# Kernel tuning notes

Hardware: AMD Instinct MI355X
Metric: run time of the kernel (lower is better)

## Reference

```python
import jax, jax.numpy as jnp
import numpy as np

C = 128                  # stem_dim
CONV_DIM = C * C * 3 * 3 # 147456
B, T = 32, 30
N_CH = 1024
N_ANS = 32               # n_answers + 1
V = 44

UNARY = [4,10,11,12,13,14,15,16,17,18,19,20,21,22,23,24,25,29,30,31,32,33,34,35,36,37,38,39,40,41,43]
BINARY = [5,6,7,8,9,26,27,28,42]
SCENE_TOK = 4

_kind = np.zeros(V, np.int32)   # 0=special, 1=scene, 2=unary, 3=binary
_uidx = np.zeros(V, np.int32)
_bidx = np.zeros(V, np.int32)
for _j, _t in enumerate(UNARY):
    _kind[_t] = 2; _uidx[_t] = _j
for _j, _t in enumerate(BINARY):
    _kind[_t] = 3; _bidx[_t] = _j
_kind[SCENE_TOK] = 1
KIND_T, U_T, B_T = jnp.array(_kind), jnp.array(_uidx), jnp.array(_bidx)


def conv3x3(x, w):  # x [N,C,H,W], w [O,I,3,3], pad=1
    return jax.lax.conv_general_dilated(x, w, (1, 1), ((1, 1), (1, 1)),
                                        dimension_numbers=('NCHW', 'OIHW', 'NCHW'))


def conv1x1(x, w):
    return jax.lax.conv_general_dilated(x, w, (1, 1), ((0, 0), (0, 0)),
                                        dimension_numbers=('NCHW', 'OIHW', 'NCHW'))

# per-sample weights: vmap conv over batch
_bconv = jax.vmap(lambda x, w: conv3x3(x[None], w)[0])


def exec_unary(x, w1, w2):
    return jax.nn.relu(_bconv(jax.nn.relu(_bconv(x, w1)), w2))


def exec_binary(x1, x2, w1, w2, w3):
    h = jax.nn.relu(_bconv(jnp.concatenate([x1, x2], axis=1), w1))
    h = jax.nn.relu(_bconv(h, w2))
    return jax.nn.relu(_bconv(h, w3))


def setup_inputs() -> dict:
    key = jax.random.key(0)
    ks = jax.random.split(key, 10)
    std = 1.0 / float(np.sqrt(CONV_DIM))
    r = lambda k, shp, s: jax.random.normal(k, shp, jnp.float32) * s
    return {
        'feats': jax.random.normal(ks[0], (B, N_CH, 14, 14), jnp.float32),
        'programs': jax.random.randint(ks[1], (B, T), 0, V, dtype=jnp.int32),
        'stem_w1': r(ks[2], (C, N_CH, 3, 3), 0.02),
        'stem_b1': jnp.zeros((C,), jnp.float32),
        'stem_w2': r(ks[3], (C, C, 3, 3), 0.05),
        'stem_b2': jnp.zeros((C,), jnp.float32),
        'mem_u': jax.random.uniform(ks[4], (31, 2 * CONV_DIM), jnp.float32, -std, std),
        'mem_b': jax.random.uniform(ks[5], (9, 4 * CONV_DIM), jnp.float32, -std, std),
        'cls_w': r(ks[6], (512, C, 1, 1), 0.05),
        'cls_b': jnp.zeros((512,), jnp.float32),
        'fc1_w': r(ks[7], (1024, 512 * 7 * 7), 0.01),
        'fc1_b': jnp.zeros((1024,), jnp.float32),
        'fc2_w': r(ks[8], (N_ANS, 1024), 0.03),
        'fc2_b': jnp.zeros((N_ANS,), jnp.float32),
    }


def reference(feats, programs, stem_w1, stem_b1, stem_w2, stem_b2, mem_u, mem_b,
              cls_w, cls_b, fc1_w, fc1_b, fc2_w, fc2_b):
    # stem: conv3x3 -> relu -> conv3x3 -> relu
    h = jax.nn.relu(conv3x3(feats, stem_w1) + stem_b1[None, :, None, None])
    feat = jax.nn.relu(conv3x3(h, stem_w2) + stem_b2[None, :, None, None])  # [B,C,14,14]

    def step(carry, tok):  # tok [B] int32
        out, saved = carry
        kind = KIND_T[tok]                           # [B]
        uread = mem_u[U_T[tok]]                      # [B, 2*CONV_DIM] one-hot memory read
        w1 = uread[:, :CONV_DIM].reshape(-1, C, C, 3, 3)
        w2 = uread[:, CONV_DIM:].reshape(-1, C, C, 3, 3)
        bread = mem_b[B_T[tok]]                      # [B, 4*CONV_DIM]
        bw1 = bread[:, :2 * CONV_DIM].reshape(-1, C, 2 * C, 3, 3)
        bw2 = bread[:, 2 * CONV_DIM:3 * CONV_DIM].reshape(-1, C, C, 3, 3)
        bw3 = bread[:, 3 * CONV_DIM:].reshape(-1, C, C, 3, 3)
        is_scene = (kind == 1)[:, None, None, None]
        u_in = jnp.where(is_scene, feat, out)        # scene runs on stem features
        u_out = exec_unary(u_in, w1, w2)
        b_out = exec_binary(out, saved, bw1, bw2, bw3)
        k4 = kind[:, None, None, None]
        new_saved = jnp.where(is_scene, out, saved)  # scene saves current output
        new_out = jnp.where(k4 == 0, out, jnp.where(k4 == 3, b_out, u_out))
        return (new_out, new_saved), None

    toks_rev = programs[:, ::-1].T.astype(jnp.int32)  # [T,B] reversed program
    (out, _), _ = jax.lax.scan(step, (feat, jnp.zeros_like(feat)), toks_rev)

    # classifier: conv1x1 -> relu -> maxpool2 -> flatten -> fc -> relu -> fc
    h = jax.nn.relu(conv1x1(out, cls_w) + cls_b[None, :, None, None])
    h = jax.lax.reduce_window(h, -jnp.inf, jax.lax.max, (1, 1, 2, 2), (1, 1, 2, 2), 'VALID')
    h = h.reshape(h.shape[0], -1)                     # [B, 512*7*7]
    h = jax.nn.relu(h @ fc1_w.T + fc1_b)
    return h @ fc2_w.T + fc2_b                        # [B, N_ANS]
```

## Files before the change

kernel.cpp:

```cpp
#include <hip/hip_runtime.h>


#define NSTEP 30
#define CD 147456
#define P 196
#define FSZ 25088
#define LROW 18
#define LBUF (272*LROW)

typedef __attribute__((ext_vector_type(8))) short short8;
typedef __attribute__((ext_vector_type(16))) float f32x16;

__constant__ int KIND_TBL[44] = {
  0,0,0,0,1,3,3,3,3,3, 2,2,2,2,2,2,2,2,2,2,
  2,2,2,2,2,2,3,3,3,2, 2,2,2,2,2,2,2,2,2,2, 2,2,3,2};
__constant__ int MIDX_TBL[44] = {
  0,0,0,0,0,0,1,2,3,4, 1,2,3,4,5,6,7,8,9,10,
  11,12,13,14,15,16,5,6,7,17, 18,19,20,21,22,23,24,25,26,27, 28,29,8,30};

__device__ __forceinline__ uint32_t bf16_rne(float x) {
  uint32_t u = __float_as_uint(x);
  return (u + 0x7fffu + ((u >> 16) & 1u)) >> 16;
}
__device__ __forceinline__ uint32_t pack_hl(float x) {
  uint32_t h = bf16_rne(x);
  float rest = x - __uint_as_float(h << 16);
  uint32_t l = bf16_rne(rest);
  return (h << 16) | l;
}
__device__ __forceinline__ float ld_sc0(const float* p) {
  return __hip_atomic_load(p, __ATOMIC_RELAXED, __HIP_MEMORY_SCOPE_AGENT);
}

__device__ __forceinline__ void bbar(int* __restrict__ ctr, int target) {
  __syncthreads();
  if (threadIdx.x == 0) {
    __hip_atomic_fetch_add(ctr, 1, __ATOMIC_RELEASE, __HIP_MEMORY_SCOPE_AGENT);
    while (__hip_atomic_load(ctr, __ATOMIC_ACQUIRE, __HIP_MEMORY_SCOPE_AGENT) < target)
      __builtin_amdgcn_s_sleep(2);
  }
  __syncthreads();
}

__global__ void __launch_bounds__(256) repack_kernel(
    const float* __restrict__ sw1, const float* __restrict__ sw2,
    const float* __restrict__ mu, const float* __restrict__ mb,
    uint32_t* __restrict__ Wp)
{
  const int blk = blockIdx.x;
  const int C = blk / 9, tap = blk % 9;
  const float* src; int nic, lc;
  if (C < 64)       { src = sw1; nic = 1024; lc = C; }
  else if (C < 72)  { src = sw2; nic = 128;  lc = C - 64; }
  else if (C < 568) { int u = (C - 72) >> 4, r = (C - 72) & 15;
                      src = mu + (size_t)u * 2 * CD + (size_t)(r >> 3) * CD;
                      nic = 128; lc = r & 7; }
  else              { int j = (C - 568) >> 5, r = (C - 568) & 31;
                      const float* base = mb + (size_t)j * 4 * CD;
                      if (r < 16)      { src = base;                  nic = 256; lc = r; }
                      else if (r < 24) { src = base + 2 * (size_t)CD; nic = 128; lc = r - 16; }
                      else             { src = base + 3 * (size_t)CD; nic = 128; lc = r - 24; } }
  const int mt = threadIdx.x >> 6, lane = threadIdx.x & 63;
  const int oc = mt * 32 + (lane & 31);
  const int ic0 = lc * 16 + (lane >> 5) * 8;
  uint32_t hw[4], lw[4];
#pragma unroll
  for (int pr = 0; pr < 4; ++pr) {
    uint32_t hh[2], ll[2];
#pragma unroll
    for (int e = 0; e < 2; ++e) {
      float x = src[((size_t)oc * nic + (ic0 + pr * 2 + e)) * 9 + tap];
      uint32_t h = bf16_rne(x);
      float rest = x - __uint_as_float(h << 16);
      hh[e] = h; ll[e] = bf16_rne(rest);
    }
    hw[pr] = hh[0] | (hh[1] << 16);
    lw[pr] = ll[0] | (ll[1] << 16);
  }
  uint32_t* dstb = Wp + (size_t)blk * 2048;
  *(uint4*)(dstb + (mt * 2 + 0) * 256 + lane * 4) = make_uint4(hw[0], hw[1], hw[2], hw[3]);
  *(uint4*)(dstb + (mt * 2 + 1) * 256 + lane * 4) = make_uint4(lw[0], lw[1], lw[2], lw[3]);
}

union BU { uint32_t u[4]; uint4 v; short8 s8; };

__device__ __forceinline__ void load_wchunk(const uint32_t* __restrict__ wb,
                                            BU* wh, BU* wl) {
#pragma unroll
  for (int t = 0; t < 9; ++t) {
    wh[t].v = *(const uint4*)(wb + t * 2048);
    wl[t].v = *(const uint4*)(wb + t * 2048 + 256);
  }
}

__device__ __forceinline__ void mfma_chunk(const uint32_t* __restrict__ sb,
                                           int pwbase, const BU* wh, const BU* wl,
                                           f32x16& acc) {
  const int TAPOFF[9] = {0, 1, 2, 16, 17, 18, 32, 33, 34};
#pragma unroll
  for (int tap = 0; tap < 9; ++tap) {
    const int pw = pwbase + TAPOFF[tap] * LROW;
    uint2 q0 = *(const uint2*)(sb + pw);
    uint2 q1 = *(const uint2*)(sb + pw + 2);
    uint2 q2 = *(const uint2*)(sb + pw + 4);
    uint2 q3 = *(const uint2*)(sb + pw + 6);
    BU Bh, Bl;
    Bh.u[0] = __builtin_amdgcn_perm(q0.y, q0.x, 0x07060302u);
    Bh.u[1] = __builtin_amdgcn_perm(q1.y, q1.x, 0x07060302u);
    Bh.u[2] = __builtin_amdgcn_perm(q2.y, q2.x, 0x07060302u);
    Bh.u[3] = __builtin_amdgcn_perm(q3.y, q3.x, 0x07060302u);
    Bl.u[0] = __builtin_amdgcn_perm(q0.y, q0.x, 0x05040100u);
    Bl.u[1] = __builtin_amdgcn_perm(q1.y, q1.x, 0x05040100u);
    Bl.u[2] = __builtin_amdgcn_perm(q2.y, q2.x, 0x05040100u);
    Bl.u[3] = __builtin_amdgcn_perm(q3.y, q3.x, 0x05040100u);
    acc = __builtin_amdgcn_mfma_f32_32x32x16_bf16(wh[tap].s8, Bh.s8, acc, 0, 0, 0);
    acc = __builtin_amdgcn_mfma_f32_32x32x16_bf16(wh[tap].s8, Bl.s8, acc, 0, 0, 0);
    acc = __builtin_amdgcn_mfma_f32_32x32x16_bf16(wl[tap].s8, Bh.s8, acc, 0, 0, 0);
  }
}

__device__ __forceinline__ void conv_run(
    uint32_t sbuf[2][LBUF],
    const float* __restrict__ in0, const float* __restrict__ in1, int split, int nc,
    int C0, int mt,
    const uint32_t* __restrict__ Wp, const float* __restrict__ bias,
    float* __restrict__ dst, float* __restrict__ dst2, float* __restrict__ zb,
    const int* imgoff)
{
  const int tid = threadIdx.x;
  const int w = tid >> 6, lane = tid & 63, l31 = lane & 31, kq = lane >> 5;
  const int ic16 = tid >> 5, pl = tid & 31;
  const int pwbase = (32 * w + l31) * LROW + kq * 8;
  const bool cw = (w < 7);
  const uint32_t* wbase = Wp + (size_t)C0 * 9 * 2048 + (mt * 2) * 256 + lane * 4;

  f32x16 acc;
#pragma unroll
  for (int i = 0; i < 16; ++i) acc[i] = 0.f;

  BU whA[9], wlA[9], whB[9], wlB[9];
  if (cw) load_wchunk(wbase, whA, wlA);
  {
    const float* src = in0 + (size_t)ic16 * P;
#pragma unroll
    for (int i = 0; i < 9; ++i) {
      int p = pl + 32 * i;
      if (p < 272) {
        int off = imgoff[i];
        float x = (off >= 0) ? ld_sc0(src + off) : 0.f;
        sbuf[0][p * LROW + ic16] = pack_hl(x);
      }
    }
  }
  __syncthreads();

  int c = 0;
  while (true) {
    {
      const bool more = c + 1 < nc;
      float sv[9];
      if (more) {
        const int cn = c + 1;
        const float* src = (cn < split) ? in0 + (size_t)(cn * 16 + ic16) * P
                                        : in1 + (size_t)((cn - split) * 16 + ic16) * P;
#pragma unroll
        for (int i = 0; i < 9; ++i) {
          int off = imgoff[i];
          sv[i] = (off >= 0) ? ld_sc0(src + off) : 0.f;
        }
        if (cw) load_wchunk(wbase + (size_t)(c + 1) * 9 * 2048, whB, wlB);
      }
      if (cw) mfma_chunk(&sbuf[c & 1][0], pwbase, whA, wlA, acc);
      if (more) {
#pragma unroll
        for (int i = 0; i < 9; ++i) {
          int p = pl + 32 * i;
          if (p < 272) sbuf[(c + 1) & 1][p * LROW + ic16] = pack_hl(sv[i]);
        }
      }
      __syncthreads();
      if (++c >= nc) break;
    }
    {
      const bool more = c + 1 < nc;
      float sv[9];
      if (more) {
        const int cn = c + 1;
        const float* src = (cn < split) ? in0 + (size_t)(cn * 16 + ic16) * P
                                        : in1 + (size_t)((cn - split) * 16 + ic16) * P;
#pragma unroll
        for (int i = 0; i < 9; ++i) {
          int off = imgoff[i];
          sv[i] = (off >= 0) ? ld_sc0(src + off) : 0.f;
        }
        if (cw) load_wchunk(wbase + (size_t)(c + 1) * 9 * 2048, whA, wlA);
      }
      if (cw) mfma_chunk(&sbuf[c & 1][0], pwbase, whB, wlB, acc);
      if (more) {
#pragma unroll
        for (int i = 0; i < 9; ++i) {
          int p = pl + 32 * i;
          if (p < 272) sbuf[(c + 1) & 1][p * LROW + ic16] = pack_hl(sv[i]);
        }
      }
      __syncthreads();
      if (++c >= nc) break;
    }
  }

  if (cw) {
    const int ox = l31 & 15, oy = 2 * w + (l31 >> 4);
    if (ox < 14) {
#pragma unroll
      for (int reg = 0; reg < 16; ++reg) {
        int row = (reg & 3) + 8 * (reg >> 2) + 4 * kq;
        int oc = mt * 32 + row;
        float v = acc[reg];
        if (bias) v += bias[row];
        v = fmaxf(v, 0.f);
        dst[(size_t)oc * P + oy * 14 + ox] = v;
        if (dst2) dst2[(size_t)oc * P + oy * 14 + ox] = v;
        if (zb)   zb[(size_t)oc * P + oy * 14 + ox] = 0.f;
      }
    }
  }
}

__global__ void __launch_bounds__(512, 2) persist_kernel(
    const float* __restrict__ feats, const int* __restrict__ progs,
    const float* __restrict__ sb1, const float* __restrict__ sb2,
    const uint32_t* __restrict__ Wp,
    float* __restrict__ feat, float* __restrict__ outb, float* __restrict__ saved,
    float* __restrict__ h1, float* __restrict__ h2, int* __restrict__ ctr)
{
  __shared__ uint32_t s_act[2][LBUF];
  const int tid = threadIdx.x;
  const int b = blockIdx.x >> 2;
  const int mt = blockIdx.x & 3;
  const size_t bo = (size_t)b * FSZ;
  int* myctr = ctr + b * 32;
  int phase = 0;

  int imgoff[9];
#pragma unroll
  for (int i = 0; i < 9; ++i) {
    int p = (tid & 31) + 32 * i;
    int row = p >> 4, col = p & 15;
    imgoff[i] = (p < 272 && row >= 1 && row <= 14 && col >= 1 && col <= 14)
                ? (row - 1) * 14 + (col - 1) : -1;
  }

  conv_run(s_act, feats + (size_t)b * 1024 * P, nullptr, 1 << 28, 64, 0, mt, Wp,
           sb1 + mt * 32, h1 + bo, nullptr, nullptr, imgoff);
  bbar(myctr, ++phase * 4);
  conv_run(s_act, h1 + bo, nullptr, 1 << 28, 8, 64, mt, Wp,
           sb2 + mt * 32, feat + bo, outb + bo, saved + bo, imgoff);
  bbar(myctr, ++phase * 4);

  for (int s = 0; s < NSTEP; ++s) {
    int tok = progs[b * NSTEP + (NSTEP - 1 - s)];
    int kind = KIND_TBL[tok], mi = MIDX_TBL[tok];
    if (kind == 0) continue;
    if (kind == 1) {
      const size_t so = bo + (size_t)mt * 32 * P;
      for (int i = tid; i < 32 * P; i += 512)
        saved[so + i] = ld_sc0(&outb[so + i]);
      int C0 = 72 + mi * 16;
      conv_run(s_act, feat + bo, nullptr, 1 << 28, 8, C0, mt, Wp, nullptr,
               h1 + bo, nullptr, nullptr, imgoff);
      bbar(myctr, ++phase * 4);
      conv_run(s_act, h1 + bo, nullptr, 1 << 28, 8, C0 + 8, mt, Wp, nullptr,
               outb + bo, nullptr, nullptr, imgoff);
      bbar(myctr, ++phase * 4);
    } else if (kind == 2) {
      int C0 = 72 + mi * 16;
      conv_run(s_act, outb + bo, nullptr, 1 << 28, 8, C0, mt, Wp, nullptr,
               h1 + bo, nullptr, nullptr, imgoff);
      bbar(myctr, ++phase * 4);
      conv_run(s_act, h1 + bo, nullptr, 1 << 28, 8, C0 + 8, mt, Wp, nullptr,
               outb + bo, nullptr, nullptr, imgoff);
      bbar(myctr, ++phase * 4);
    } else {
      int C0 = 568 + mi * 32;
      conv_run(s_act, outb + bo, saved + bo, 8, 16, C0, mt, Wp, nullptr,
               h1 + bo, nullptr, nullptr, imgoff);
      bbar(myctr, ++phase * 4);
      conv_run(s_act, h1 + bo, nullptr, 1 << 28, 8, C0 + 16, mt, Wp, nullptr,
               h2 + bo, nullptr, nullptr, imgoff);
      bbar(myctr, ++phase * 4);
      conv_run(s_act, h2 + bo, nullptr, 1 << 28, 8, C0 + 24, mt, Wp, nullptr,
               outb + bo, nullptr, nullptr, imgoff);
      bbar(myctr, ++phase * 4);
    }
  }
}

__global__ void __launch_bounds__(256) cls_pool_kernel(
    const float* __restrict__ x, const float* __restrict__ Wc,
    const float* __restrict__ bc, float* __restrict__ hB)
{
  const int b = blockIdx.y, og = blockIdx.x;
  const int oc0 = og * 64;
  __shared__ float s[16 * P];
  const float* xb = x + (size_t)b * FSZ;
  const int tid = threadIdx.x;
  float acc[13][4];
#pragma unroll
  for (int k = 0; k < 13; ++k) { acc[k][0] = acc[k][1] = acc[k][2] = acc[k][3] = 0.f; }
  for (int c0 = 0; c0 < 128; c0 += 16) {
    __syncthreads();
    for (int i = tid; i < 16 * P; i += 256) s[i] = xb[(size_t)c0 * P + i];
    __syncthreads();
#pragma unroll
    for (int k = 0; k < 13; ++k) {
      const int idx = k * 256 + tid;
      if (idx < 64 * 49) {
        const int oc = oc0 + idx / 49, pp = idx % 49;
        const int py = pp / 7, px = pp % 7;
        const int b0 = 2 * py * 14 + 2 * px, b1 = b0 + 14;
        const float* wr = Wc + (size_t)oc * 128 + c0;
#pragma unroll
        for (int ic = 0; ic < 16; ++ic) {
          const float w = wr[ic];
          const float* sp = s + ic * P;
          const float2 r0 = *(const float2*)(sp + b0);
          const float2 r1 = *(const float2*)(sp + b1);
          acc[k][0] = fmaf(w, r0.x, acc[k][0]);
          acc[k][1] = fmaf(w, r0.y, acc[k][1]);
          acc[k][2] = fmaf(w, r1.x, acc[k][2]);
          acc[k][3] = fmaf(w, r1.y, acc[k][3]);
        }
      }
    }
  }
#pragma unroll
  for (int k = 0; k < 13; ++k) {
    const int idx = k * 256 + tid;
    if (idx < 64 * 49) {
      const int oc = oc0 + idx / 49, pp = idx % 49;
      const float m = fmaxf(fmaxf(acc[k][0], acc[k][1]), fmaxf(acc[k][2], acc[k][3]));
      hB[(size_t)b * 25088 + (size_t)oc * 49 + pp] = fmaxf(m + bc[oc], 0.f);
    }
  }
}

__global__ void __launch_bounds__(256) transpose_kernel(
    const float* __restrict__ hB, float* __restrict__ hT)
{
  __shared__ float t[256 * 33];
  const int k0 = blockIdx.x * 256;
  const int tid = threadIdx.x;
  for (int b = 0; b < 32; ++b)
    t[tid * 33 + b] = hB[(size_t)b * 25088 + k0 + tid];
  __syncthreads();
  for (int i = tid; i < 256 * 32; i += 256) {
    const int k = i >> 5, b = i & 31;
    hT[(size_t)(k0 + k) * 32 + b] = t[k * 33 + b];
  }
}

__global__ void __launch_bounds__(256) fc1_kernel(
    const float* __restrict__ hT, const float* __restrict__ W,
    const float* __restrict__ bias, float* __restrict__ o)
{
  const int b = threadIdx.x & 31, j = threadIdx.x >> 5;
  const int oc = blockIdx.x * 4 + (j & 3);
  const int kh = j >> 2;
  const float* wr = W + (size_t)oc * 25088 + (size_t)kh * 12544;
  const float* ht = hT + (size_t)kh * 12544 * 32;
  float acc = 0.f;
  for (int k = 0; k < 12544; k += 4) {
    const float4 w4 = *(const float4*)(wr + k);
    acc = fmaf(ht[(size_t)(k + 0) * 32 + b], w4.x, acc);
    acc = fmaf(ht[(size_t)(k + 1) * 32 + b], w4.y, acc);
    acc = fmaf(ht[(size_t)(k + 2) * 32 + b], w4.z, acc);
    acc = fmaf(ht[(size_t)(k + 3) * 32 + b], w4.w, acc);
  }
  __shared__ float red[8][32];
  red[j][b] = acc;
  __syncthreads();
  if (j < 4)
    o[(size_t)b * 1024 + oc] = fmaxf(red[j][b] + red[j + 4][b] + bias[oc], 0.f);
}

__global__ void __launch_bounds__(256) fc2_kernel(
    const float* __restrict__ h, const float* __restrict__ W,
    const float* __restrict__ bias, float* __restrict__ out)
{
  const int i = blockIdx.x * 256 + threadIdx.x;
  const int b = i >> 5, oo = i & 31;
  const float* wr = W + (size_t)oo * 1024;
  const float* hr = h + (size_t)b * 1024;
  float acc = bias[oo];
  for (int k = 0; k < 1024; k += 4) {
    const float4 w4 = *(const float4*)(wr + k);
    const float4 h4 = *(const float4*)(hr + k);
    acc = fmaf(h4.x, w4.x, acc);
    acc = fmaf(h4.y, w4.y, acc);
    acc = fmaf(h4.z, w4.z, acc);
    acc = fmaf(h4.w, w4.w, acc);
  }
  out[i] = acc;
}

extern "C" void kernel_launch(void* const* d_in, const int* in_sizes, int n_in,
                              void* d_out, int out_size, void* d_ws, size_t ws_size,
                              hipStream_t stream) {
  const float* feats   = (const float*)d_in[0];
  const int*   progs   = (const int*)  d_in[1];
  const float* stem_w1 = (const float*)d_in[2];
  const float* stem_b1 = (const float*)d_in[3];
  const float* stem_w2 = (const float*)d_in[4];
  const float* stem_b2 = (const float*)d_in[5];
  const float* mem_u   = (const float*)d_in[6];
  const float* mem_b   = (const float*)d_in[7];
  const float* cls_w   = (const float*)d_in[8];
  const float* cls_b   = (const float*)d_in[9];
  const float* fc1_w   = (const float*)d_in[10];
  const float* fc1_b   = (const float*)d_in[11];
  const float* fc2_w   = (const float*)d_in[12];
  const float* fc2_b   = (const float*)d_in[13];

  float* ws = (float*)d_ws;
  const size_t F = (size_t)32 * FSZ;
  float*    feat  = ws;
  float*    outb  = ws + 1 * F;
  float*    saved = ws + 2 * F;
  float*    h1    = ws + 3 * F;
  float*    h2    = ws + 4 * F;
  uint32_t* Wp    = (uint32_t*)(ws + 5 * F);
  int*      ctr   = (int*)(Wp + (size_t)7704 * 2048);

  hipMemsetAsync(ctr, 0, 32 * 32 * sizeof(int), stream);

  repack_kernel<<<dim3(7704), dim3(256), 0, stream>>>(stem_w1, stem_w2, mem_u, mem_b, Wp);

  persist_kernel<<<dim3(128), dim3(512), 0, stream>>>(
      feats, progs, stem_b1, stem_b2, Wp, feat, outb, saved, h1, h2, ctr);

  float* hB   = h1;
  float* hT   = h2;
  float* fc1o = saved;
  cls_pool_kernel<<<dim3(8, 32), dim3(256), 0, stream>>>(outb, cls_w, cls_b, hB);
  transpose_kernel<<<dim3(98), dim3(256), 0, stream>>>(hB, hT);
  fc1_kernel<<<dim3(256), dim3(256), 0, stream>>>(hT, fc1_w, fc1_b, fc1o);
  fc2_kernel<<<dim3(4), dim3(256), 0, stream>>>(fc1o, fc2_w, fc2_b, (float*)d_out);
}
```

Before: 3.354 ms.

## Split conv input channels across two blocks with deferred sum and ReLU

```diff
diff --git a/kernel.cpp b/kernel.cpp
--- a/kernel.cpp
+++ b/kernel.cpp
@@ -36,8 +36,9 @@
   __syncthreads();
   if (threadIdx.x == 0) {
     __hip_atomic_fetch_add(ctr, 1, __ATOMIC_RELEASE, __HIP_MEMORY_SCOPE_AGENT);
-    while (__hip_atomic_load(ctr, __ATOMIC_ACQUIRE, __HIP_MEMORY_SCOPE_AGENT) < target)
+    while (__hip_atomic_load(ctr, __ATOMIC_RELAXED, __HIP_MEMORY_SCOPE_AGENT) < target)
       __builtin_amdgcn_s_sleep(2);
+    (void)__hip_atomic_load(ctr, __ATOMIC_ACQUIRE, __HIP_MEMORY_SCOPE_AGENT);
   }
   __syncthreads();
 }
@@ -119,9 +120,51 @@
   }
 }
 
+template<int MODE>
+__device__ __forceinline__ void stage_load(
+    const float* __restrict__ in0A, const float* __restrict__ in0B,
+    const float* __restrict__ in1A, const float* __restrict__ in1B,
+    int split, int cn, int ic16, const int* imgoff, float* sv)
+{
+  if (MODE == 0) {
+    const float* sA = in0A + (size_t)(cn * 16 + ic16) * P;
+#pragma unroll
+    for (int i = 0; i < 9; ++i) {
+      int off = imgoff[i];
+      sv[i] = (off >= 0) ? sA[off] : 0.f;
+    }
+  } else if (MODE == 1) {
+    size_t o = (size_t)(cn * 16 + ic16) * P;
+    const float* sA = in0A + o;
+    const float* sB = in0B + o;
+#pragma unroll
+    for (int i = 0; i < 9; ++i) {
+      int off = imgoff[i];
+      sv[i] = (off >= 0) ? fmaxf(ld_sc0(sA + off) + ld_sc0(sB + off), 0.f) : 0.f;
+    }
+  } else {
+    const float* sA; const float* sB;
+    if (cn < split) {
+      size_t o = (size_t)(cn * 16 + ic16) * P;
+      sA = in0A + o; sB = in0B + o;
+    } else {
+      size_t o = (size_t)((cn - split) * 16 + ic16) * P;
+      sA = in1A + o; sB = in1B + o;
+    }
+#pragma unroll
+    for (int i = 0; i < 9; ++i) {
+      int off = imgoff[i];
+      sv[i] = (off >= 0) ? fmaxf(ld_sc0(sA + off) + ld_sc0(sB + off), 0.f) : 0.f;
+    }
+  }
+}
+
+template<int MODE>
 __device__ __forceinline__ void conv_run(
     uint32_t sbuf[2][LBUF],
-    const float* __restrict__ in0, const float* __restrict__ in1, int split, int nc,
+    const float* __restrict__ in0A, const float* __restrict__ in0B,
+    const float* __restrict__ in1A, const float* __restrict__ in1B,
+    int split, int cbeg, int n,
     int C0, int mt,
     const uint32_t* __restrict__ Wp, const float* __restrict__ bias,
     float* __restrict__ dst, float* __restrict__ dst2, float* __restrict__ zb,
@@ -139,72 +182,55 @@
   for (int i = 0; i < 16; ++i) acc[i] = 0.f;
 
   BU whA[9], wlA[9], whB[9], wlB[9];
-  if (cw) load_wchunk(wbase, whA, wlA);
+  if (cw) load_wchunk(wbase + (size_t)cbeg * 9 * 2048, whA, wlA);
   {
-    const float* src = in0 + (size_t)ic16 * P;
+    float sv[9];
+    stage_load<MODE>(in0A, in0B, in1A, in1B, split, cbeg, ic16, imgoff, sv);
 #pragma unroll
     for (int i = 0; i < 9; ++i) {
       int p = pl + 32 * i;
-      if (p < 272) {
-        int off = imgoff[i];
-        float x = (off >= 0) ? ld_sc0(src + off) : 0.f;
-        sbuf[0][p * LROW + ic16] = pack_hl(x);
-      }
+      if (p < 272) sbuf[0][p * LROW + ic16] = pack_hl(sv[i]);
     }
   }
   __syncthreads();
 
-  int c = 0;
+  int k = 0;
   while (true) {
     {
-      const bool more = c + 1 < nc;
+      const bool more = (k + 1 < n);
       float sv[9];
       if (more) {
-        const int cn = c + 1;
-        const float* src = (cn < split) ? in0 + (size_t)(cn * 16 + ic16) * P
-                                        : in1 + (size_t)((cn - split) * 16 + ic16) * P;
-#pragma unroll
-        for (int i = 0; i < 9; ++i) {
-          int off = imgoff[i];
-          sv[i] = (off >= 0) ? ld_sc0(src + off) : 0.f;
-        }
-        if (cw) load_wchunk(wbase + (size_t)(c + 1) * 9 * 2048, whB, wlB);
-      }
-      if (cw) mfma_chunk(&sbuf[c & 1][0], pwbase, whA, wlA, acc);
+        stage_load<MODE>(in0A, in0B, in1A, in1B, split, cbeg + k + 1, ic16, imgoff, sv);
+        if (cw) load_wchunk(wbase + (size_t)(cbeg + k + 1) * 9 * 2048, whB, wlB);
+      }
+      if (cw) mfma_chunk(&sbuf[k & 1][0], pwbase, whA, wlA, acc);
       if (more) {
 #pragma unroll
         for (int i = 0; i < 9; ++i) {
           int p = pl + 32 * i;
-          if (p < 272) sbuf[(c + 1) & 1][p * LROW + ic16] = pack_hl(sv[i]);
+          if (p < 272) sbuf[(k + 1) & 1][p * LROW + ic16] = pack_hl(sv[i]);
         }
       }
       __syncthreads();
-      if (++c >= nc) break;
+      if (++k >= n) break;
     }
     {
-      const bool more = c + 1 < nc;
+      const bool more = (k + 1 < n);
       float sv[9];
       if (more) {
-        const int cn = c + 1;
-        const float* src = (cn < split) ? in0 + (size_t)(cn * 16 + ic16) * P
-                                        : in1 + (size_t)((cn - split) * 16 + ic16) * P;
-#pragma unroll
-        for (int i = 0; i < 9; ++i) {
-          int off = imgoff[i];
-          sv[i] = (off >= 0) ? ld_sc0(src + off) : 0.f;
-        }
-        if (cw) load_wchunk(wbase + (size_t)(c + 1) * 9 * 2048, whA, wlA);
-      }
-      if (cw) mfma_chunk(&sbuf[c & 1][0], pwbase, whB, wlB, acc);
+        stage_load<MODE>(in0A, in0B, in1A, in1B, split, cbeg + k + 1, ic16, imgoff, sv);
+        if (cw) load_wchunk(wbase + (size_t)(cbeg + k + 1) * 9 * 2048, whA, wlA);
+      }
+      if (cw) mfma_chunk(&sbuf[k & 1][0], pwbase, whB, wlB, acc);
       if (more) {
 #pragma unroll
         for (int i = 0; i < 9; ++i) {
           int p = pl + 32 * i;
-          if (p < 272) sbuf[(c + 1) & 1][p * LROW + ic16] = pack_hl(sv[i]);
+          if (p < 272) sbuf[(k + 1) & 1][p * LROW + ic16] = pack_hl(sv[i]);
         }
       }
       __syncthreads();
-      if (++c >= nc) break;
+      if (++k >= n) break;
     }
   }
 
@@ -217,7 +243,6 @@
         int oc = mt * 32 + row;
         float v = acc[reg];
         if (bias) v += bias[row];
-        v = fmaxf(v, 0.f);
         dst[(size_t)oc * P + oy * 14 + ox] = v;
         if (dst2) dst2[(size_t)oc * P + oy * 14 + ox] = v;
         if (zb)   zb[(size_t)oc * P + oy * 14 + ox] = 0.f;
@@ -226,20 +251,34 @@
   }
 }
 
-__global__ void __launch_bounds__(512, 2) persist_kernel(
+__global__ void __launch_bounds__(512, 1) persist_kernel(
     const float* __restrict__ feats, const int* __restrict__ progs,
     const float* __restrict__ sb1, const float* __restrict__ sb2,
     const uint32_t* __restrict__ Wp,
-    float* __restrict__ feat, float* __restrict__ outb, float* __restrict__ saved,
-    float* __restrict__ h1, float* __restrict__ h2, int* __restrict__ ctr)
+    float* __restrict__ featA, float* __restrict__ featB,
+    float* __restrict__ outbA, float* __restrict__ outbB,
+    float* __restrict__ savedA, float* __restrict__ savedB,
+    float* __restrict__ h1A, float* __restrict__ h1B,
+    float* __restrict__ h2A, float* __restrict__ h2B,
+    int* __restrict__ ctr)
 {
   __shared__ uint32_t s_act[2][LBUF];
   const int tid = threadIdx.x;
-  const int b = blockIdx.x >> 2;
-  const int mt = blockIdx.x & 3;
+  const int b = blockIdx.x & 31;
+  const int slice = blockIdx.x >> 5;
+  const int mt = slice & 3;
+  const int kh = slice >> 2;
   const size_t bo = (size_t)b * FSZ;
   int* myctr = ctr + b * 32;
   int phase = 0;
+
+  float* featP  = kh ? featB  : featA;
+  float* outbP  = kh ? outbB  : outbA;
+  float* savedP = kh ? savedB : savedA;
+  float* h1P    = kh ? h1B    : h1A;
+  float* h2P    = kh ? h2B    : h2A;
+  const float* bias1 = kh ? nullptr : sb1 + mt * 32;
+  const float* bias2 = kh ? nullptr : sb2 + mt * 32;
 
   int imgoff[9];
 #pragma unroll
@@ -250,12 +289,14 @@
                 ? (row - 1) * 14 + (col - 1) : -1;
   }
 
-  conv_run(s_act, feats + (size_t)b * 1024 * P, nullptr, 1 << 28, 64, 0, mt, Wp,
-           sb1 + mt * 32, h1 + bo, nullptr, nullptr, imgoff);
-  bbar(myctr, ++phase * 4);
-  conv_run(s_act, h1 + bo, nullptr, 1 << 28, 8, 64, mt, Wp,
-           sb2 + mt * 32, feat + bo, outb + bo, saved + bo, imgoff);
-  bbar(myctr, ++phase * 4);
+  conv_run<0>(s_act, feats + (size_t)b * 1024 * P, nullptr, nullptr, nullptr,
+              1 << 28, kh * 32, 32, 0, mt, Wp, bias1,
+              h1P + bo, nullptr, nullptr, imgoff);
+  bbar(myctr, ++phase * 8);
+  conv_run<1>(s_act, h1A + bo, h1B + bo, nullptr, nullptr, 1 << 28,
+              kh * 4, 4, 64, mt, Wp, bias2,
+              featP + bo, outbP + bo, savedP + bo, imgoff);
+  bbar(myctr, ++phase * 8);
 
   for (int s = 0; s < NSTEP; ++s) {
     int tok = progs[b * NSTEP + (NSTEP - 1 - s)];
@@ -264,52 +305,55 @@
     if (kind == 1) {
       const size_t so = bo + (size_t)mt * 32 * P;
       for (int i = tid; i < 32 * P; i += 512)
-        saved[so + i] = ld_sc0(&outb[so + i]);
+        savedP[so + i] = outbP[so + i];
       int C0 = 72 + mi * 16;
-      conv_run(s_act, feat + bo, nullptr, 1 << 28, 8, C0, mt, Wp, nullptr,
-               h1 + bo, nullptr, nullptr, imgoff);
-      bbar(myctr, ++phase * 4);
-      conv_run(s_act, h1 + bo, nullptr, 1 << 28, 8, C0 + 8, mt, Wp, nullptr,
-               outb + bo, nullptr, nullptr, imgoff);
-      bbar(myctr, ++phase * 4);
+      conv_run<1>(s_act, featA + bo, featB + bo, nullptr, nullptr, 1 << 28,
+                  kh * 4, 4, C0, mt, Wp, nullptr, h1P + bo, nullptr, nullptr, imgoff);
+      bbar(myctr, ++phase * 8);
+      conv_run<1>(s_act, h1A + bo, h1B + bo, nullptr, nullptr, 1 << 28,
+                  kh * 4, 4, C0 + 8, mt, Wp, nullptr, outbP + bo, nullptr, nullptr, imgoff);
+      bbar(myctr, ++phase * 8);
     } else if (kind == 2) {
       int C0 = 72 + mi * 16;
-      conv_run(s_act, outb + bo, nullptr, 1 << 28, 8, C0, mt, Wp, nullptr,
-               h1 + bo, nullptr, nullptr, imgoff);
-      bbar(myctr, ++phase * 4);
-      conv_run(s_act, h1 + bo, nullptr, 1 << 28, 8, C0 + 8, mt, Wp, nullptr,
-               outb + bo, nullptr, nullptr, imgoff);
-      bbar(myctr, ++phase * 4);
+      conv_run<1>(s_act, outbA + bo, outbB + bo, nullptr, nullptr, 1 << 28,
+                  kh * 4, 4, C0, mt, Wp, nullptr, h1P + bo, nullptr, nullptr, imgoff);
+      bbar(myctr, ++phase * 8);
+      conv_run<1>(s_act, h1A + bo, h1B + bo, nullptr, nullptr, 1 << 28,
+                  kh * 4, 4, C0 + 8, mt, Wp, nullptr, outbP + bo, nullptr, nullptr, imgoff);
+      bbar(myctr, ++phase * 8);
     } else {
       int C0 = 568 + mi * 32;
-      conv_run(s_act, outb + bo, saved + bo, 8, 16, C0, mt, Wp, nullptr,
-               h1 + bo, nullptr, nullptr, imgoff);
-      bbar(myctr, ++phase * 4);
-      conv_run(s_act, h1 + bo, nullptr, 1 << 28, 8, C0 + 16, mt, Wp, nullptr,
-               h2 + bo, nullptr, nullptr, imgoff);
-      bbar(myctr, ++phase * 4);
-      conv_run(s_act, h2 + bo, nullptr, 1 << 28, 8, C0 + 24, mt, Wp, nullptr,
-               outb + bo, nullptr, nullptr, imgoff);
-      bbar(myctr, ++phase * 4);
+      conv_run<2>(s_act, outbA + bo, outbB + bo, savedA + bo, savedB + bo, 8,
+                  kh * 8, 8, C0, mt, Wp, nullptr, h1P + bo, nullptr, nullptr, imgoff);
+      bbar(myctr, ++phase * 8);
+      conv_run<1>(s_act, h1A + bo, h1B + bo, nullptr, nullptr, 1 << 28,
+                  kh * 4, 4, C0 + 16, mt, Wp, nullptr, h2P + bo, nullptr, nullptr, imgoff);
+      bbar(myctr, ++phase * 8);
+      conv_run<1>(s_act, h2A + bo, h2B + bo, nullptr, nullptr, 1 << 28,
+                  kh * 4, 4, C0 + 24, mt, Wp, nullptr, outbP + bo, nullptr, nullptr, imgoff);
+      bbar(myctr, ++phase * 8);
     }
   }
 }
 
 __global__ void __launch_bounds__(256) cls_pool_kernel(
-    const float* __restrict__ x, const float* __restrict__ Wc,
-    const float* __restrict__ bc, float* __restrict__ hB)
+    const float* __restrict__ xA, const float* __restrict__ xB,
+    const float* __restrict__ Wc, const float* __restrict__ bc,
+    float* __restrict__ hB)
 {
   const int b = blockIdx.y, og = blockIdx.x;
   const int oc0 = og * 64;
   __shared__ float s[16 * P];
-  const float* xb = x + (size_t)b * FSZ;
+  const float* xbA = xA + (size_t)b * FSZ;
+  const float* xbB = xB + (size_t)b * FSZ;
   const int tid = threadIdx.x;
   float acc[13][4];
 #pragma unroll
   for (int k = 0; k < 13; ++k) { acc[k][0] = acc[k][1] = acc[k][2] = acc[k][3] = 0.f; }
   for (int c0 = 0; c0 < 128; c0 += 16) {
     __syncthreads();
-    for (int i = tid; i < 16 * P; i += 256) s[i] = xb[(size_t)c0 * P + i];
+    for (int i = tid; i < 16 * P; i += 256)
+      s[i] = fmaxf(xbA[(size_t)c0 * P + i] + xbB[(size_t)c0 * P + i], 0.f);
     __syncthreads();
 #pragma unroll
     for (int k = 0; k < 13; ++k) {
@@ -423,25 +467,31 @@
 
   float* ws = (float*)d_ws;
   const size_t F = (size_t)32 * FSZ;
-  float*    feat  = ws;
-  float*    outb  = ws + 1 * F;
-  float*    saved = ws + 2 * F;
-  float*    h1    = ws + 3 * F;
-  float*    h2    = ws + 4 * F;
-  uint32_t* Wp    = (uint32_t*)(ws + 5 * F);
+  float*    featA  = ws + 0 * F;
+  float*    featB  = ws + 1 * F;
+  float*    outbA  = ws + 2 * F;
+  float*    outbB  = ws + 3 * F;
+  float*    savedA = ws + 4 * F;
+  float*    savedB = ws + 5 * F;
+  float*    h1A    = ws + 6 * F;
+  float*    h1B    = ws + 7 * F;
+  float*    h2A    = ws + 8 * F;
+  float*    h2B    = ws + 9 * F;
+  uint32_t* Wp    = (uint32_t*)(ws + 10 * F);
   int*      ctr   = (int*)(Wp + (size_t)7704 * 2048);
 
   hipMemsetAsync(ctr, 0, 32 * 32 * sizeof(int), stream);
 
   repack_kernel<<<dim3(7704), dim3(256), 0, stream>>>(stem_w1, stem_w2, mem_u, mem_b, Wp);
 
-  persist_kernel<<<dim3(128), dim3(512), 0, stream>>>(
-      feats, progs, stem_b1, stem_b2, Wp, feat, outb, saved, h1, h2, ctr);
-
-  float* hB   = h1;
-  float* hT   = h2;
-  float* fc1o = saved;
-  cls_pool_kernel<<<dim3(8, 32), dim3(256), 0, stream>>>(outb, cls_w, cls_b, hB);
+  persist_kernel<<<dim3(256), dim3(512), 0, stream>>>(
+      feats, progs, stem_b1, stem_b2, Wp,
+      featA, featB, outbA, outbB, savedA, savedB, h1A, h1B, h2A, h2B, ctr);
+
+  float* hB   = h1A;
+  float* hT   = h2A;
+  float* fc1o = savedA;
+  cls_pool_kernel<<<dim3(8, 32), dim3(256), 0, stream>>>(outbA, outbB, cls_w, cls_b, hB);
   transpose_kernel<<<dim3(98), dim3(256), 0, stream>>>(hB, hT);
   fc1_kernel<<<dim3(256), dim3(256), 0, stream>>>(hT, fc1_w, fc1_b, fc1o);
   fc2_kernel<<<dim3(4), dim3(256), 0, stream>>>(fc1o, fc2_w, fc2_b, (float*)d_out);
```

Result: no change. 3.388 ms (+1.0%).

## Process each sample in one 1024-thread block, removing cross-block barriers

Applied to the files above, without the earlier changes.

```diff
diff --git a/kernel.cpp b/kernel.cpp
--- a/kernel.cpp
+++ b/kernel.cpp
@@ -27,19 +27,6 @@
   float rest = x - __uint_as_float(h << 16);
   uint32_t l = bf16_rne(rest);
   return (h << 16) | l;
-}
-__device__ __forceinline__ float ld_sc0(const float* p) {
-  return __hip_atomic_load(p, __ATOMIC_RELAXED, __HIP_MEMORY_SCOPE_AGENT);
-}
-
-__device__ __forceinline__ void bbar(int* __restrict__ ctr, int target) {
-  __syncthreads();
-  if (threadIdx.x == 0) {
-    __hip_atomic_fetch_add(ctr, 1, __ATOMIC_RELEASE, __HIP_MEMORY_SCOPE_AGENT);
-    while (__hip_atomic_load(ctr, __ATOMIC_ACQUIRE, __HIP_MEMORY_SCOPE_AGENT) < target)
-      __builtin_amdgcn_s_sleep(2);
-  }
-  __syncthreads();
 }
 
 __global__ void __launch_bounds__(256) repack_kernel(
@@ -84,162 +71,148 @@
 
 union BU { uint32_t u[4]; uint4 v; short8 s8; };
 
-__device__ __forceinline__ void load_wchunk(const uint32_t* __restrict__ wb,
-                                            BU* wh, BU* wl) {
-#pragma unroll
-  for (int t = 0; t < 9; ++t) {
-    wh[t].v = *(const uint4*)(wb + t * 2048);
-    wl[t].v = *(const uint4*)(wb + t * 2048 + 256);
-  }
-}
-
-__device__ __forceinline__ void mfma_chunk(const uint32_t* __restrict__ sb,
-                                           int pwbase, const BU* wh, const BU* wl,
-                                           f32x16& acc) {
+__device__ __forceinline__ void mfma_tap(const uint32_t* __restrict__ sb, int pw,
+                                         const BU& wh, const BU& wl, f32x16& acc) {
+  uint2 q0 = *(const uint2*)(sb + pw);
+  uint2 q1 = *(const uint2*)(sb + pw + 2);
+  uint2 q2 = *(const uint2*)(sb + pw + 4);
+  uint2 q3 = *(const uint2*)(sb + pw + 6);
+  BU Bh, Bl;
+  Bh.u[0] = __builtin_amdgcn_perm(q0.y, q0.x, 0x07060302u);
+  Bh.u[1] = __builtin_amdgcn_perm(q1.y, q1.x, 0x07060302u);
+  Bh.u[2] = __builtin_amdgcn_perm(q2.y, q2.x, 0x07060302u);
+  Bh.u[3] = __builtin_amdgcn_perm(q3.y, q3.x, 0x07060302u);
+  Bl.u[0] = __builtin_amdgcn_perm(q0.y, q0.x, 0x05040100u);
+  Bl.u[1] = __builtin_amdgcn_perm(q1.y, q1.x, 0x05040100u);
+  Bl.u[2] = __builtin_amdgcn_perm(q2.y, q2.x, 0x05040100u);
+  Bl.u[3] = __builtin_amdgcn_perm(q3.y, q3.x, 0x05040100u);
+  acc = __builtin_amdgcn_mfma_f32_32x32x16_bf16(wh.s8, Bh.s8, acc, 0, 0, 0);
+  acc = __builtin_amdgcn_mfma_f32_32x32x16_bf16(wh.s8, Bl.s8, acc, 0, 0, 0);
+  acc = __builtin_amdgcn_mfma_f32_32x32x16_bf16(wl.s8, Bh.s8, acc, 0, 0, 0);
+}
+
+__device__ __forceinline__ void chunk_compute(const uint32_t* __restrict__ sb,
+                                              int pwb, const uint32_t* __restrict__ wc,
+                                              int pq, f32x16& a0, f32x16& a1) {
   const int TAPOFF[9] = {0, 1, 2, 16, 17, 18, 32, 33, 34};
-#pragma unroll
-  for (int tap = 0; tap < 9; ++tap) {
-    const int pw = pwbase + TAPOFF[tap] * LROW;
-    uint2 q0 = *(const uint2*)(sb + pw);
-    uint2 q1 = *(const uint2*)(sb + pw + 2);
-    uint2 q2 = *(const uint2*)(sb + pw + 4);
-    uint2 q3 = *(const uint2*)(sb + pw + 6);
-    BU Bh, Bl;
-    Bh.u[0] = __builtin_amdgcn_perm(q0.y, q0.x, 0x07060302u);
-    Bh.u[1] = __builtin_amdgcn_perm(q1.y, q1.x, 0x07060302u);
-    Bh.u[2] = __builtin_amdgcn_perm(q2.y, q2.x, 0x07060302u);
-    Bh.u[3] = __builtin_amdgcn_perm(q3.y, q3.x, 0x07060302u);
-    Bl.u[0] = __builtin_amdgcn_perm(q0.y, q0.x, 0x05040100u);
-    Bl.u[1] = __builtin_amdgcn_perm(q1.y, q1.x, 0x05040100u);
-    Bl.u[2] = __builtin_amdgcn_perm(q2.y, q2.x, 0x05040100u);
-    Bl.u[3] = __builtin_amdgcn_perm(q3.y, q3.x, 0x05040100u);
-    acc = __builtin_amdgcn_mfma_f32_32x32x16_bf16(wh[tap].s8, Bh.s8, acc, 0, 0, 0);
-    acc = __builtin_amdgcn_mfma_f32_32x32x16_bf16(wh[tap].s8, Bl.s8, acc, 0, 0, 0);
-    acc = __builtin_amdgcn_mfma_f32_32x32x16_bf16(wl[tap].s8, Bh.s8, acc, 0, 0, 0);
-  }
-}
-
-__device__ __forceinline__ void conv_run(
-    uint32_t sbuf[2][LBUF],
-    const float* __restrict__ in0, const float* __restrict__ in1, int split, int nc,
-    int C0, int mt,
-    const uint32_t* __restrict__ Wp, const float* __restrict__ bias,
+  const int g0 = 2 * pq;
+  const bool g1v = (g0 + 1 < 7);
+#pragma unroll
+  for (int tg = 0; tg < 3; ++tg) {
+    BU wh[3], wl[3];
+#pragma unroll
+    for (int t = 0; t < 3; ++t) {
+      wh[t].v = *(const uint4*)(wc + (tg * 3 + t) * 2048);
+      wl[t].v = *(const uint4*)(wc + (tg * 3 + t) * 2048 + 256);
+    }
+#pragma unroll
+    for (int t = 0; t < 3; ++t) {
+      const int off = TAPOFF[tg * 3 + t];
+      mfma_tap(sb, pwb + (32 * g0 + off) * LROW, wh[t], wl[t], a0);
+      if (g1v)
+        mfma_tap(sb, pwb + (32 * (g0 + 1) + off) * LROW, wh[t], wl[t], a1);
+    }
+  }
+}
+
+template<int MODE>
+__device__ __forceinline__ void stage_load(
+    const float* __restrict__ in0, const float* __restrict__ in1,
+    int cn, int ic16, const int* imgoff, float* sv)
+{
+  const float* s;
+  if (MODE == 0) s = in0 + (size_t)(cn * 16 + ic16) * P;
+  else s = (cn < 8) ? in0 + (size_t)(cn * 16 + ic16) * P
+                    : in1 + (size_t)((cn - 8) * 16 + ic16) * P;
+#pragma unroll
+  for (int i = 0; i < 9; ++i) {
+    int off = imgoff[i];
+    sv[i] = (off >= 0) ? s[off] : 0.f;
+  }
+}
+
+__device__ __forceinline__ void lds_write_chunk(uint32_t* __restrict__ sb,
+                                                int pl, int ic16, const float* sv) {
+#pragma unroll
+  for (int i = 0; i < 9; ++i) {
+    int p = pl + 32 * i;
+    if (p < 272) sb[p * LROW + ic16] = pack_hl(sv[i]);
+  }
+}
+
+template<int MODE>
+__device__ __forceinline__ void conv_full(
+    uint32_t (*sbuf)[LBUF],
+    const float* __restrict__ in0, const float* __restrict__ in1, int npair,
+    int C0, const uint32_t* __restrict__ Wp, const float* __restrict__ bias,
     float* __restrict__ dst, float* __restrict__ dst2, float* __restrict__ zb,
     const int* imgoff)
 {
   const int tid = threadIdx.x;
-  const int w = tid >> 6, lane = tid & 63, l31 = lane & 31, kq = lane >> 5;
-  const int ic16 = tid >> 5, pl = tid & 31;
-  const int pwbase = (32 * w + l31) * LROW + kq * 8;
-  const bool cw = (w < 7);
+  const int lane = tid & 63, l31 = lane & 31, kq = lane >> 5;
+  const int w = tid >> 6;
+  const int mt = w & 3, pq = w >> 2;
+  const int ic16 = (tid >> 5) & 15, pl = tid & 31, half = tid >> 9;
+  const int pwb = l31 * LROW + kq * 8;
   const uint32_t* wbase = Wp + (size_t)C0 * 9 * 2048 + (mt * 2) * 256 + lane * 4;
 
-  f32x16 acc;
-#pragma unroll
-  for (int i = 0; i < 16; ++i) acc[i] = 0.f;
-
-  BU whA[9], wlA[9], whB[9], wlB[9];
-  if (cw) load_wchunk(wbase, whA, wlA);
-  {
-    const float* src = in0 + (size_t)ic16 * P;
-#pragma unroll
-    for (int i = 0; i < 9; ++i) {
-      int p = pl + 32 * i;
-      if (p < 272) {
-        int off = imgoff[i];
-        float x = (off >= 0) ? ld_sc0(src + off) : 0.f;
-        sbuf[0][p * LROW + ic16] = pack_hl(x);
-      }
-    }
-  }
+  f32x16 a0, a1;
+#pragma unroll
+  for (int i = 0; i < 16; ++i) { a0[i] = 0.f; a1[i] = 0.f; }
+
+  float sv[9];
+  stage_load<MODE>(in0, in1, half, ic16, imgoff, sv);
+  lds_write_chunk(&sbuf[half][0], pl, ic16, sv);
   __syncthreads();
 
-  int c = 0;
-  while (true) {
-    {
-      const bool more = c + 1 < nc;
-      float sv[9];
-      if (more) {
-        const int cn = c + 1;
-        const float* src = (cn < split) ? in0 + (size_t)(cn * 16 + ic16) * P
-                                        : in1 + (size_t)((cn - split) * 16 + ic16) * P;
-#pragma unroll
-        for (int i = 0; i < 9; ++i) {
-          int off = imgoff[i];
-          sv[i] = (off >= 0) ? ld_sc0(src + off) : 0.f;
-        }
-        if (cw) load_wchunk(wbase + (size_t)(c + 1) * 9 * 2048, whB, wlB);
-      }
-      if (cw) mfma_chunk(&sbuf[c & 1][0], pwbase, whA, wlA, acc);
-      if (more) {
-#pragma unroll
-        for (int i = 0; i < 9; ++i) {
-          int p = pl + 32 * i;
-          if (p < 272) sbuf[(c + 1) & 1][p * LROW + ic16] = pack_hl(sv[i]);
+  for (int p = 0; p < npair; ++p) {
+    const bool more = (p + 1 < npair);
+    if (more)
+      stage_load<MODE>(in0, in1, 2 * (p + 1) + half, ic16, imgoff, sv);
+    const uint32_t* wp0 = wbase + (size_t)(2 * p) * 9 * 2048;
+    chunk_compute(&sbuf[(p & 1) * 2 + 0][0], pwb, wp0,            pq, a0, a1);
+    chunk_compute(&sbuf[(p & 1) * 2 + 1][0], pwb, wp0 + 9 * 2048, pq, a0, a1);
+    if (more)
+      lds_write_chunk(&sbuf[((p + 1) & 1) * 2 + half][0], pl, ic16, sv);
+    __syncthreads();
+  }
+
+#pragma unroll
+  for (int gi = 0; gi < 2; ++gi) {
+    const int g = 2 * pq + gi;
+    if (g < 7) {
+      const int px = 32 * g + l31;
+      const int oy = px >> 4, ox = px & 15;
+      if (ox < 14) {
+        const f32x16& a = gi ? a1 : a0;
+#pragma unroll
+        for (int reg = 0; reg < 16; ++reg) {
+          int row = (reg & 3) + 8 * (reg >> 2) + 4 * kq;
+          int oc = mt * 32 + row;
+          float v = a[reg];
+          if (bias) v += bias[oc];
+          v = fmaxf(v, 0.f);
+          dst[(size_t)oc * P + oy * 14 + ox] = v;
+          if (dst2) dst2[(size_t)oc * P + oy * 14 + ox] = v;
+          if (zb)   zb[(size_t)oc * P + oy * 14 + ox] = 0.f;
         }
       }
-      __syncthreads();
-      if (++c >= nc) break;
-    }
-    {
-      const bool more = c + 1 < nc;
-      float sv[9];
-      if (more) {
-        const int cn = c + 1;
-        const float* src = (cn < split) ? in0 + (size_t)(cn * 16 + ic16) * P
-                                        : in1 + (size_t)((cn - split) * 16 + ic16) * P;
-#pragma unroll
-        for (int i = 0; i < 9; ++i) {
-          int off = imgoff[i];
-          sv[i] = (off >= 0) ? ld_sc0(src + off) : 0.f;
-        }
-        if (cw) load_wchunk(wbase + (size_t)(c + 1) * 9 * 2048, whA, wlA);
-      }
-      if (cw) mfma_chunk(&sbuf[c & 1][0], pwbase, whB, wlB, acc);
-      if (more) {
-#pragma unroll
-        for (int i = 0; i < 9; ++i) {
-          int p = pl + 32 * i;
-          if (p < 272) sbuf[(c + 1) & 1][p * LROW + ic16] = pack_hl(sv[i]);
-        }
-      }
-      __syncthreads();
-      if (++c >= nc) break;
-    }
-  }
-
-  if (cw) {
-    const int ox = l31 & 15, oy = 2 * w + (l31 >> 4);
-    if (ox < 14) {
-#pragma unroll
-      for (int reg = 0; reg < 16; ++reg) {
-        int row = (reg & 3) + 8 * (reg >> 2) + 4 * kq;
-        int oc = mt * 32 + row;
-        float v = acc[reg];
-        if (bias) v += bias[row];
-        v = fmaxf(v, 0.f);
-        dst[(size_t)oc * P + oy * 14 + ox] = v;
-        if (dst2) dst2[(size_t)oc * P + oy * 14 + ox] = v;
-        if (zb)   zb[(size_t)oc * P + oy * 14 + ox] = 0.f;
-      }
-    }
-  }
-}
-
-__global__ void __launch_bounds__(512, 2) persist_kernel(
+    }
+  }
+  __syncthreads();
+}
+
+__global__ void __launch_bounds__(1024) persist_kernel(
     const float* __restrict__ feats, const int* __restrict__ progs,
     const float* __restrict__ sb1, const float* __restrict__ sb2,
     const uint32_t* __restrict__ Wp,
     float* __restrict__ feat, float* __restrict__ outb, float* __restrict__ saved,
-    float* __restrict__ h1, float* __restrict__ h2, int* __restrict__ ctr)
-{
-  __shared__ uint32_t s_act[2][LBUF];
+    float* __restrict__ h1, float* __restrict__ h2)
+{
+  __shared__ uint32_t s_act[4][LBUF];
   const int tid = threadIdx.x;
-  const int b = blockIdx.x >> 2;
-  const int mt = blockIdx.x & 3;
+  const int b = blockIdx.x;
   const size_t bo = (size_t)b * FSZ;
-  int* myctr = ctr + b * 32;
-  int phase = 0;
 
   int imgoff[9];
 #pragma unroll
@@ -250,47 +223,38 @@
                 ? (row - 1) * 14 + (col - 1) : -1;
   }
 
-  conv_run(s_act, feats + (size_t)b * 1024 * P, nullptr, 1 << 28, 64, 0, mt, Wp,
-           sb1 + mt * 32, h1 + bo, nullptr, nullptr, imgoff);
-  bbar(myctr, ++phase * 4);
-  conv_run(s_act, h1 + bo, nullptr, 1 << 28, 8, 64, mt, Wp,
-           sb2 + mt * 32, feat + bo, outb + bo, saved + bo, imgoff);
-  bbar(myctr, ++phase * 4);
+  conv_full<0>(s_act, feats + (size_t)b * 1024 * P, nullptr, 32, 0, Wp,
+               sb1, h1 + bo, nullptr, nullptr, imgoff);
+  conv_full<0>(s_act, h1 + bo, nullptr, 4, 64, Wp,
+               sb2, feat + bo, outb + bo, saved + bo, imgoff);
 
   for (int s = 0; s < NSTEP; ++s) {
     int tok = progs[b * NSTEP + (NSTEP - 1 - s)];
     int kind = KIND_TBL[tok], mi = MIDX_TBL[tok];
     if (kind == 0) continue;
     if (kind == 1) {
-      const size_t so = bo + (size_t)mt * 32 * P;
-      for (int i = tid; i < 32 * P; i += 512)
-        saved[so + i] = ld_sc0(&outb[so + i]);
+      for (int i = tid; i < FSZ; i += 1024)
+        saved[bo + i] = outb[bo + i];
+      __syncthreads();
       int C0 = 72 + mi * 16;
-      conv_run(s_act, feat + bo, nullptr, 1 << 28, 8, C0, mt, Wp, nullptr,
-               h1 + bo, nullptr, nullptr, imgoff);
-      bbar(myctr, ++phase * 4);
-      conv_run(s_act, h1 + bo, nullptr, 1 << 28, 8, C0 + 8, mt, Wp, nullptr,
-               outb + bo, nullptr, nullptr, imgoff);
-      bbar(myctr, ++phase * 4);
+      conv_full<0>(s_act, feat + bo, nullptr, 4, C0, Wp, nullptr,
+                   h1 + bo, nullptr, nullptr, imgoff);
+      conv_full<0>(s_act, h1 + bo, nullptr, 4, C0 + 8, Wp, nullptr,
+                   outb + bo, nullptr, nullptr, imgoff);
     } else if (kind == 2) {
       int C0 = 72 + mi * 16;
-      conv_run(s_act, outb + bo, nullptr, 1 << 28, 8, C0, mt, Wp, nullptr,
-               h1 + bo, nullptr, nullptr, imgoff);
-      bbar(myctr, ++phase * 4);
-      conv_run(s_act, h1 + bo, nullptr, 1 << 28, 8, C0 + 8, mt, Wp, nullptr,
-               outb + bo, nullptr, nullptr, imgoff);
-      bbar(myctr, ++phase * 4);
+      conv_full<0>(s_act, outb + bo, nullptr, 4, C0, Wp, nullptr,
+                   h1 + bo, nullptr, nullptr, imgoff);
+      conv_full<0>(s_act, h1 + bo, nullptr, 4, C0 + 8, Wp, nullptr,
+                   outb + bo, nullptr, nullptr, imgoff);
     } else {
       int C0 = 568 + mi * 32;
-      conv_run(s_act, outb + bo, saved + bo, 8, 16, C0, mt, Wp, nullptr,
-               h1 + bo, nullptr, nullptr, imgoff);
-      bbar(myctr, ++phase * 4);
-      conv_run(s_act, h1 + bo, nullptr, 1 << 28, 8, C0 + 16, mt, Wp, nullptr,
-               h2 + bo, nullptr, nullptr, imgoff);
-      bbar(myctr, ++phase * 4);
-      conv_run(s_act, h2 + bo, nullptr, 1 << 28, 8, C0 + 24, mt, Wp, nullptr,
-               outb + bo, nullptr, nullptr, imgoff);
-      bbar(myctr, ++phase * 4);
+      conv_full<2>(s_act, outb + bo, saved + bo, 8, C0, Wp, nullptr,
+                   h1 + bo, nullptr, nullptr, imgoff);
+      conv_full<0>(s_act, h1 + bo, nullptr, 4, C0 + 16, Wp, nullptr,
+                   h2 + bo, nullptr, nullptr, imgoff);
+      conv_full<0>(s_act, h2 + bo, nullptr, 4, C0 + 24, Wp, nullptr,
+                   outb + bo, nullptr, nullptr, imgoff);
     }
   }
 }
@@ -423,20 +387,17 @@
 
   float* ws = (float*)d_ws;
   const size_t F = (size_t)32 * FSZ;
-  float*    feat  = ws;
+  float*    feat  = ws + 0 * F;
   float*    outb  = ws + 1 * F;
   float*    saved = ws + 2 * F;
   float*    h1    = ws + 3 * F;
   float*    h2    = ws + 4 * F;
   uint32_t* Wp    = (uint32_t*)(ws + 5 * F);
-  int*      ctr   = (int*)(Wp + (size_t)7704 * 2048);
-
-  hipMemsetAsync(ctr, 0, 32 * 32 * sizeof(int), stream);
 
   repack_kernel<<<dim3(7704), dim3(256), 0, stream>>>(stem_w1, stem_w2, mem_u, mem_b, Wp);
 
-  persist_kernel<<<dim3(128), dim3(512), 0, stream>>>(
-      feats, progs, stem_b1, stem_b2, Wp, feat, outb, saved, h1, h2, ctr);
+  persist_kernel<<<dim3(32), dim3(1024), 0, stream>>>(
+      feats, progs, stem_b1, stem_b2, Wp, feat, outb, saved, h1, h2);
 
   float* hB   = h1;
   float* hT   = h2;
```

Result: slower. 5.145 ms (+53.4%).
